# Kernel tuning notes

Measured on AMD Instinct MI355X. Metric: run time of the kernel, lower is better.

The kernel has to match this reference:

```python
import jax, jax.numpy as jnp
import numpy as np

N = 50000      # nodes
E = 300000     # edges per hop
H = 64         # hidden_channels
P = 3          # hops
DIRS = 3
L = 2          # num_layers
G = 50         # graphs in batch
FUS_IN = H * (2 + 2 * DIRS)  # 512
SLOPE = 0.01   # torch leaky_relu default negative slope


def setup_inputs():
    key = jax.random.key(0)
    ks = jax.random.split(key, 32)
    def nrm(k, shape, s=0.1):
        return jax.random.normal(k, shape, jnp.float32) * s
    return {
        "x": jax.random.normal(ks[0], (N, H), jnp.float32),
        "pe": jax.random.normal(ks[1], (N, DIRS), jnp.float32),
        "batch": jnp.sort(jax.random.randint(ks[2], (N,), 0, G, jnp.int32)),
        "u_edge_index": jax.random.randint(ks[3], (P, 2, E), 0, N, jnp.int32),
        "u_edge_weight": jax.random.uniform(ks[4], (P, E), jnp.float32),
        "f_edge_index": jax.random.randint(ks[5], (P, 2, E), 0, N, jnp.int32),
        "f_edge_weight": jax.random.uniform(ks[6], (P, E), jnp.float32),
        "emb_W": nrm(ks[7], (H, H)), "emb_b": nrm(ks[8], (H,)),
        "S_lin_W": nrm(ks[9], (L, H, H)), "S_lin_b": nrm(ks[10], (L, H)),
        "S_d": nrm(ks[11], (L, P, H), 1.0), "S_hb": nrm(ks[12], (L, P, H)),
        "S_fW": nrm(ks[13], (L, P, FUS_IN, H), 0.04), "S_fb": nrm(ks[14], (L, P, H)),
        "F_lin_W": nrm(ks[15], (L, H, H)), "F_lin_b": nrm(ks[16], (L, H)),
        "F_d": nrm(ks[17], (L, P, H), 1.0), "F_hb": nrm(ks[18], (L, P, H)),
        "F_fW": nrm(ks[19], (L, P, FUS_IN, H), 0.04), "F_fb": nrm(ks[20], (L, P, H)),
        "nS_w": 1.0 + nrm(ks[21], (L, H)), "nS_b": nrm(ks[22], (L, H)),
        "nS_m": 1.0 + nrm(ks[23], (L, H)),
        "nF_w": 1.0 + nrm(ks[24], (L, H)), "nF_b": nrm(ks[25], (L, H)),
        "nF_m": 1.0 + nrm(ks[26], (L, H)),
        "gate_W": nrm(ks[27], (2 * H, H)), "gate_b": nrm(ks[28], (H,)),
    }


def _opdmp(x, pe, ei, ew, lin_W, lin_b, d, hop_bias, fus_W, fus_b):
    """One OPDMPConv: multi-hop gather / scatter_add with directional weights."""
    x_t = x @ lin_W + lin_b              # [N, H]
    d_w = jax.nn.softmax(d, axis=0)      # [P, H]
    out = jnp.zeros_like(x_t)
    u = pe[:, :DIRS]
    for p in range(P):
        row, col, w = ei[p, 0], ei[p, 1], ew[p]
        # precompute() runs under torch.no_grad() -> stop_gradient
        deg = jax.ops.segment_sum(jax.lax.stop_gradient(w), row, num_segments=N)
        deg_inv = jnp.where(deg == 0.0, 0.0, 1.0 / deg)                  # [N]
        diff = jax.lax.stop_gradient(u[col] - u[row])                    # [E, DIRS]
        W2 = jnp.concatenate([jax.nn.relu(diff), jax.nn.relu(-diff)], axis=1)  # [E, 2*DIRS]
        xc = x_t[col]                                                    # [E, H] gather
        out_avg = jax.ops.segment_sum(xc * w[:, None], row, num_segments=N) * deg_inv[:, None]
        msg_dir = (xc[:, :, None] * W2[:, None, :]).reshape(E, H * 2 * DIRS)
        out_dir = jax.ops.segment_sum(msg_dir, row, num_segments=N) * deg_inv[:, None]
        h_cat = jnp.concatenate([x_t, out_avg, out_dir], axis=-1)        # [N, FUS_IN]
        h_p = jax.nn.leaky_relu(h_cat @ fus_W[p] + fus_b[p], SLOPE)
        out = out + h_p * d_w[p] + hop_bias[p]
    return out


def _graph_norm(x, batch, w, b, ms):
    cnt = jnp.maximum(jax.ops.segment_sum(jnp.ones((N,), x.dtype), batch, num_segments=G), 1.0)
    mean = jax.ops.segment_sum(x, batch, num_segments=G) / cnt[:, None]
    out = x - mean[batch] * ms
    var = jax.ops.segment_sum(out * out, batch, num_segments=G) / cnt[:, None]
    return out / jnp.sqrt(var[batch] + 1e-5) * w + b


def _forward(x, pe, u_edge_weight, f_edge_weight, emb_W, emb_b,
             S_lin_W, S_lin_b, S_d, S_hb, S_fW, S_fb,
             F_lin_W, F_lin_b, F_d, F_hb, F_fW, F_fb,
             nS_w, nS_b, nS_m, nF_w, nF_b, nF_m,
             gate_W, gate_b, batch, u_edge_index, f_edge_index):
    x = x @ emb_W + emb_b
    for i in range(L):
        prev = x
        h = _opdmp(x, pe, u_edge_index, u_edge_weight,
                   S_lin_W[i], S_lin_b[i], S_d[i], S_hb[i], S_fW[i], S_fb[i])
        h = jax.nn.leaky_relu(_graph_norm(h, batch, nS_w[i], nS_b[i], nS_m[i]), SLOPE)
        fx = _opdmp(h, pe, f_edge_index, f_edge_weight,
                    F_lin_W[i], F_lin_b[i], F_d[i], F_hb[i], F_fW[i], F_fb[i])
        fx = jax.nn.leaky_relu(_graph_norm(fx, batch, nF_w[i], nF_b[i], nF_m[i]), SLOPE)
        gate = jax.nn.sigmoid(jnp.concatenate([h, fx], axis=-1) @ gate_W + gate_b)
        x = gate * h + (1.0 - gate) * fx + prev   # dropout = identity in eval mode
    cnt = jnp.maximum(jax.ops.segment_sum(jnp.ones((N,), x.dtype), batch, num_segments=G), 1.0)
    return jax.ops.segment_sum(x, batch, num_segments=G) / cnt[:, None]  # global_mean_pool


def reference(x, pe, batch, u_edge_index, u_edge_weight, f_edge_index, f_edge_weight,
              emb_W, emb_b, S_lin_W, S_lin_b, S_d, S_hb, S_fW, S_fb,
              F_lin_W, F_lin_b, F_d, F_hb, F_fW, F_fb,
              nS_w, nS_b, nS_m, nF_w, nF_b, nF_m, gate_W, gate_b):
    return _forward(x, pe, u_edge_weight, f_edge_weight, emb_W, emb_b,
                    S_lin_W, S_lin_b, S_d, S_hb, S_fW, S_fb,
                    F_lin_W, F_lin_b, F_d, F_hb, F_fW, F_fb,
                    nS_w, nS_b, nS_m, nF_w, nF_b, nF_m,
                    gate_W, gate_b, batch, u_edge_index, f_edge_index)
```

## Files before the change

kernel.cpp:

```cpp
#include <hip/hip_runtime.h>
#include <cstdint>
#include <cstddef>

#define NN 50000
#define EE 300000
#define HH 64
#define PP 3
#define GG 50
#define LL 2
#define CAP 32
#define SLOPE 0.01f

typedef __attribute__((ext_vector_type(8))) short bf16x8;
typedef __attribute__((ext_vector_type(4))) float f32x4;

__device__ __forceinline__ float lrelu(float x){ return x >= 0.f ? x : SLOPE*x; }

__device__ __forceinline__ unsigned short f2bf(float x){
    uint32_t u = __float_as_uint(x);
    uint32_t r = (u + 0x7FFFu + ((u >> 16) & 1u)) >> 16;
    return (unsigned short)r;
}
__device__ __forceinline__ float bf2f(unsigned short s){
    return __uint_as_float((uint32_t)s << 16);
}

__global__ void k_bounds(const int* __restrict__ batch, int* __restrict__ gstart){
    int g = threadIdx.x;
    if (g > GG) return;
    int lo = 0, hi = NN;
    while (lo < hi){ int mid = (lo + hi) >> 1; if (batch[mid] < g) lo = mid + 1; else hi = mid; }
    gstart[g] = lo;
}

__global__ void k_pe4(const float* __restrict__ pe, float4* __restrict__ pe4){
    int n = blockIdx.x * blockDim.x + threadIdx.x;
    if (n >= NN) return;
    pe4[n] = make_float4(pe[n * 3 + 0], pe[n * 3 + 1], pe[n * 3 + 2], 0.f);
}

__global__ void k_fill2(const int* __restrict__ uei, const float* __restrict__ uew,
                        const int* __restrict__ fei, const float* __restrict__ few,
                        int* __restrict__ cnt, int2* __restrict__ bucket){
    int t = blockIdx.x * blockDim.x + threadIdx.x;
    if (t >= 2 * PP * EE) return;
    int which = t / EE;
    int e = t - which * EE;
    const int* ei; const float* ew; int p;
    if (which < PP){ ei = uei; ew = uew; p = which; }
    else           { ei = fei; ew = few; p = which - PP; }
    int row = ei[(size_t)(p * 2 + 0) * EE + e];
    int col = ei[(size_t)(p * 2 + 1) * EE + e];
    float w = ew[(size_t)p * EE + e];
    int slot = atomicAdd(cnt + (size_t)which * NN + row, 1);
    if (slot < CAP)
        bucket[((size_t)which * NN + row) * CAP + slot] = make_int2(col, __float_as_int(w));
}

__global__ void k_wpermb(const float* __restrict__ S_fW, const float* __restrict__ F_fW,
                         unsigned short* __restrict__ Wpb){
    int gid = blockIdx.x * blockDim.x + threadIdx.x;
    int j = gid & 7;
    int lane = (gid >> 3) & 63;
    int w = (gid >> 9) & 3;
    int kb = (gid >> 11) & 15;
    int t = gid >> 15;
    int q = kb * 32 + (lane >> 4) * 8 + j;
    int col = w * 16 + (lane & 15);
    int conv = t / 6, layer = (t % 6) / 3, p = t % 3;
    const float* src = (conv ? F_fW : S_fW) + ((size_t)layer * PP + p) * 512 * HH;
    int kref;
    if (q < 128) kref = q;
    else { int r = q - 128; kref = 128 + (r & 63) * 6 + (r >> 6); }
    Wpb[gid] = f2bf(src[(size_t)kref * HH + col]);
}

__global__ __launch_bounds__(256) void k_lin64(const float* __restrict__ X,
                       const float* __restrict__ W, const float* __restrict__ b,
                       float* __restrict__ out){
    __shared__ float xs[32][HH];
    int nb = blockIdx.x * 32;
    int t = threadIdx.x;
    #pragma unroll
    for (int i = 0; i < 2; ++i){
        int idx = t + 256 * i;
        int r = idx >> 4, c4 = idx & 15;
        int n = nb + r;
        float4 v = make_float4(0.f, 0.f, 0.f, 0.f);
        if (n < NN) v = *reinterpret_cast<const float4*>(X + (size_t)n * HH + c4 * 4);
        *reinterpret_cast<float4*>(&xs[r][c4 * 4]) = v;
    }
    __syncthreads();
    int lane = t & 63, wave = t >> 6, nw = wave * 8;
    float acc[8];
    float bb = b[lane];
    #pragma unroll
    for (int i = 0; i < 8; ++i) acc[i] = bb;
    #pragma unroll 2
    for (int k = 0; k < HH; ++k){
        float wv = W[(size_t)k * HH + lane];
        #pragma unroll
        for (int i = 0; i < 8; ++i) acc[i] += xs[nw + i][k] * wv;
    }
    #pragma unroll
    for (int i = 0; i < 8; ++i){
        int n = nb + nw + i;
        if (n < NN) out[(size_t)n * HH + lane] = acc[i];
    }
}

__global__ __launch_bounds__(256) void k_lin64b(const float* __restrict__ X,
                       const float* __restrict__ W, const float* __restrict__ b,
                       unsigned short* __restrict__ out){
    __shared__ float xs[32][HH];
    int nb = blockIdx.x * 32;
    int t = threadIdx.x;
    #pragma unroll
    for (int i = 0; i < 2; ++i){
        int idx = t + 256 * i;
        int r = idx >> 4, c4 = idx & 15;
        int n = nb + r;
        float4 v = make_float4(0.f, 0.f, 0.f, 0.f);
        if (n < NN) v = *reinterpret_cast<const float4*>(X + (size_t)n * HH + c4 * 4);
        *reinterpret_cast<float4*>(&xs[r][c4 * 4]) = v;
    }
    __syncthreads();
    int lane = t & 63, wave = t >> 6, nw = wave * 8;
    float acc[8];
    float bb = b[lane];
    #pragma unroll
    for (int i = 0; i < 8; ++i) acc[i] = bb;
    #pragma unroll 2
    for (int k = 0; k < HH; ++k){
        float wv = W[(size_t)k * HH + lane];
        #pragma unroll
        for (int i = 0; i < 8; ++i) acc[i] += xs[nw + i][k] * wv;
    }
    #pragma unroll
    for (int i = 0; i < 8; ++i){
        int n = nb + nw + i;
        if (n < NN) out[(size_t)n * HH + lane] = f2bf(acc[i]);
    }
}

__global__ __launch_bounds__(256) void k_hop3(const unsigned short* __restrict__ xtb,
        const int* __restrict__ cnt, const int2* __restrict__ bucket,
        const float4* __restrict__ pe4, const unsigned short* __restrict__ Wpb3,
        const float* __restrict__ fb3, const float* __restrict__ dmat,
        const float* __restrict__ hb3, float* __restrict__ outb){
    __shared__ unsigned short u[16][512];
    int nb = blockIdx.x * 16;
    int t = threadIdx.x;
    int lane = t & 63, wave = t >> 6, nw = wave * 4;
    {
        int r = t >> 4, c4 = t & 15;
        ushort4 s = *reinterpret_cast<const ushort4*>(xtb + (size_t)(nb + r) * HH + c4 * 4);
        int q = (c4 * 4) ^ ((r & 7) << 3);
        *reinterpret_cast<ushort4*>(&u[r][q]) = s;
    }
    int c = wave * 16 + (lane & 15);
    float d0 = dmat[c], d1 = dmat[64 + c], d2 = dmat[128 + c];
    float mx = fmaxf(d0, fmaxf(d1, d2));
    float e0 = expf(d0 - mx), e1 = expf(d1 - mx), e2 = expf(d2 - mx);
    float esum = e0 + e1 + e2;
    float dw0 = e0 / esum, dw1 = e1 / esum, dw2 = e2 / esum;
    float accOut[4];
    float hbs = hb3[c] + hb3[64 + c] + hb3[128 + c];
    #pragma unroll
    for (int r = 0; r < 4; ++r) accOut[r] = hbs;

    for (int p = 0; p < 3; ++p){
        __syncthreads();
        const int*  cntp = cnt + (size_t)p * NN;
        const int2* bp   = bucket + (size_t)p * NN * CAP;
        #pragma unroll
        for (int i = 0; i < 4; ++i){
            int n = nb + nw + i;
            float accA = 0.f, sumw = 0.f;
            float a0 = 0.f, a1 = 0.f, a2 = 0.f, a3 = 0.f, a4 = 0.f, a5 = 0.f;
            int len = cntp[n]; if (len > CAP) len = CAP;
            const int2* b = bp + (size_t)n * CAP;
            float4 pr = pe4[n];
            {
                int  cols[8]; float ws[8];
                #pragma unroll
                for (int s = 0; s < 8; ++s){
                    int2 m = b[s];
                    bool ok = (s < len);
                    cols[s] = ok ? m.x : n;
                    ws[s]   = ok ? __int_as_float(m.y) : 0.f;
                }
                float4 pcs[8]; float xvs[8];
                #pragma unroll
                for (int s = 0; s < 8; ++s){
                    pcs[s] = pe4[cols[s]];
                    xvs[s] = bf2f(xtb[(size_t)cols[s] * HH + lane]);
                }
                #pragma unroll
                for (int s = 0; s < 8; ++s){
                    float w = ws[s], xv = xvs[s];
                    float dd0 = pcs[s].x - pr.x;
                    float dd1 = pcs[s].y - pr.y;
                    float dd2 = pcs[s].z - pr.z;
                    sumw += w;  accA += w * xv;
                    a0 += fmaxf(dd0, 0.f) * xv;  a3 += fmaxf(-dd0, 0.f) * xv;
                    a1 += fmaxf(dd1, 0.f) * xv;  a4 += fmaxf(-dd1, 0.f) * xv;
                    a2 += fmaxf(dd2, 0.f) * xv;  a5 += fmaxf(-dd2, 0.f) * xv;
                }
            }
            if (len > 8){
                int  cols[8]; float ws[8];
                #pragma unroll
                for (int s = 0; s < 8; ++s){
                    int2 m = b[8 + s];
                    bool ok = (8 + s < len);
                    cols[s] = ok ? m.x : n;
                    ws[s]   = ok ? __int_as_float(m.y) : 0.f;
                }
                float4 pcs[8]; float xvs[8];
                #pragma unroll
                for (int s = 0; s < 8; ++s){
                    pcs[s] = pe4[cols[s]];
                    xvs[s] = bf2f(xtb[(size_t)cols[s] * HH + lane]);
                }
                #pragma unroll
                for (int s = 0; s < 8; ++s){
                    float w = ws[s], xv = xvs[s];
                    float dd0 = pcs[s].x - pr.x;
                    float dd1 = pcs[s].y - pr.y;
                    float dd2 = pcs[s].z - pr.z;
                    sumw += w;  accA += w * xv;
                    a0 += fmaxf(dd0, 0.f) * xv;  a3 += fmaxf(-dd0, 0.f) * xv;
                    a1 += fmaxf(dd1, 0.f) * xv;  a4 += fmaxf(-dd1, 0.f) * xv;
                    a2 += fmaxf(dd2, 0.f) * xv;  a5 += fmaxf(-dd2, 0.f) * xv;
                }
            }
            for (int s = 16; s < len; ++s){
                int2 m = b[s];
                int col = m.x;
                float w = __int_as_float(m.y);
                float4 pc = pe4[col];
                float xv = bf2f(xtb[(size_t)col * HH + lane]);
                float dd0 = pc.x - pr.x;
                float dd1 = pc.y - pr.y;
                float dd2 = pc.z - pr.z;
                sumw += w;  accA += w * xv;
                a0 += fmaxf(dd0, 0.f) * xv;  a3 += fmaxf(-dd0, 0.f) * xv;
                a1 += fmaxf(dd1, 0.f) * xv;  a4 += fmaxf(-dd1, 0.f) * xv;
                a2 += fmaxf(dd2, 0.f) * xv;  a5 += fmaxf(-dd2, 0.f) * xv;
            }
            float di = (sumw == 0.f) ? 0.f : 1.f / sumw;
            int il = nw + i;
            int sw = (il & 7) << 3;
            u[il][(64 + lane) ^ sw]           = f2bf(accA * di);
            u[il][(128 + 0 * 64 + lane) ^ sw] = f2bf(a0 * di);
            u[il][(128 + 1 * 64 + lane) ^ sw] = f2bf(a1 * di);
            u[il][(128 + 2 * 64 + lane) ^ sw] = f2bf(a2 * di);
            u[il][(128 + 3 * 64 + lane) ^ sw] = f2bf(a3 * di);
            u[il][(128 + 4 * 64 + lane) ^ sw] = f2bf(a4 * di);
            u[il][(128 + 5 * 64 + lane) ^ sw] = f2bf(a5 * di);
        }
        __syncthreads();
        const unsigned short* wb = Wpb3 + (size_t)p * 32768;
        f32x4 acc = {0.f, 0.f, 0.f, 0.f};
        int arow = lane & 15;
        int asw = (arow & 7) << 3;
        #pragma unroll
        for (int kb = 0; kb < 16; ++kb){
            int qa = (kb * 32 + (lane >> 4) * 8) ^ asw;
            bf16x8 a = *reinterpret_cast<const bf16x8*>(&u[arow][qa]);
            bf16x8 b = *reinterpret_cast<const bf16x8*>(&wb[(((size_t)kb * 4 + wave) * 64 + lane) * 8]);
            acc = __builtin_amdgcn_mfma_f32_16x16x32_bf16(a, b, acc, 0, 0, 0);
        }
        float fbv = fb3[p * 64 + c];
        float dw = (p == 0) ? dw0 : ((p == 1) ? dw1 : dw2);
        #pragma unroll
        for (int r = 0; r < 4; ++r)
            accOut[r] += lrelu(acc[r] + fbv) * dw;
    }
    #pragma unroll
    for (int r = 0; r < 4; ++r){
        int row = (lane >> 4) * 4 + r;
        outb[(size_t)(nb + row) * HH + c] = accOut[r];
    }
}

__global__ void k_stats4(const float* __restrict__ X, const int* __restrict__ gstart,
                         float* __restrict__ sums4, float* __restrict__ sumsq4){
    int g = blockIdx.x, chunk = blockIdx.y;
    int o = threadIdx.x & 63, sub = threadIdx.x >> 6;
    int ns = gstart[g], ne = gstart[g + 1];
    float s = 0.f, q = 0.f;
    for (int n = ns + chunk * 4 + sub; n < ne; n += 16){
        float v = X[(size_t)n * 64 + o];
        s += v; q += v * v;
    }
    __shared__ float ls[4][64];
    __shared__ float lq[4][64];
    ls[sub][o] = s; lq[sub][o] = q;
    __syncthreads();
    if (sub == 0){
        #pragma unroll
        for (int k = 1; k < 4; ++k){ s += ls[k][o]; q += lq[k][o]; }
        sums4 [(size_t)(chunk * GG + g) * 64 + o] = s;
        sumsq4[(size_t)(chunk * GG + g) * 64 + o] = q;
    }
}

__global__ void k_gnorm(float* __restrict__ X, const int* __restrict__ batch,
                        const int* __restrict__ gstart,
                        const float* __restrict__ sums4, const float* __restrict__ sumsq4,
                        const float* __restrict__ w, const float* __restrict__ b,
                        const float* __restrict__ ms){
    int gid = blockIdx.x * blockDim.x + threadIdx.x;
    if (gid >= NN * HH) return;
    int n = gid >> 6, o = gid & 63;
    int g = batch[n];
    float cnt = fmaxf((float)(gstart[g + 1] - gstart[g]), 1.f);
    float sm = 0.f, sq = 0.f;
    #pragma unroll
    for (int cC = 0; cC < 4; ++cC){
        sm += sums4 [(size_t)(cC * GG + g) * 64 + o];
        sq += sumsq4[(size_t)(cC * GG + g) * 64 + o];
    }
    float mean = sm / cnt;
    float ex2 = sq / cnt;
    float m = ms[o];
    float var = ex2 - mean * mean * m * (2.f - m);
    float v = (X[gid] - mean * m) * (1.f / sqrtf(var + 1e-5f)) * w[o] + b[o];
    X[gid] = lrelu(v);
}

__global__ __launch_bounds__(256) void k_gate2(const float* __restrict__ h,
                       const float* __restrict__ fx, const float* __restrict__ gW,
                       const float* __restrict__ gb, float* __restrict__ X){
    __shared__ float hs[32][HH];
    __shared__ float fs[32][HH];
    int nb = blockIdx.x * 32;
    int t = threadIdx.x;
    #pragma unroll
    for (int i = 0; i < 2; ++i){
        int idx = t + 256 * i;
        int r = idx >> 4, c4 = idx & 15;
        int n = nb + r;
        float4 vh = make_float4(0.f, 0.f, 0.f, 0.f);
        float4 vf = make_float4(0.f, 0.f, 0.f, 0.f);
        if (n < NN){
            vh = *reinterpret_cast<const float4*>(h  + (size_t)n * HH + c4 * 4);
            vf = *reinterpret_cast<const float4*>(fx + (size_t)n * HH + c4 * 4);
        }
        *reinterpret_cast<float4*>(&hs[r][c4 * 4]) = vh;
        *reinterpret_cast<float4*>(&fs[r][c4 * 4]) = vf;
    }
    __syncthreads();
    int lane = t & 63, wave = t >> 6, nw = wave * 8;
    float acc[8];
    float bb = gb[lane];
    #pragma unroll
    for (int i = 0; i < 8; ++i) acc[i] = bb;
    #pragma unroll 2
    for (int k = 0; k < HH; ++k){
        float w1 = gW[(size_t)k * HH + lane];
        float w2 = gW[(size_t)(64 + k) * HH + lane];
        #pragma unroll
        for (int i = 0; i < 8; ++i) acc[i] += hs[nw + i][k] * w1 + fs[nw + i][k] * w2;
    }
    #pragma unroll
    for (int i = 0; i < 8; ++i){
        int n = nb + nw + i;
        if (n < NN){
            float gt = 1.f / (1.f + expf(-acc[i]));
            float hv = hs[nw + i][lane];
            float fv = fs[nw + i][lane];
            size_t idx = (size_t)n * HH + lane;
            X[idx] = gt * hv + (1.f - gt) * fv + X[idx];
        }
    }
}

__global__ void k_finalout(const float* __restrict__ sums4, const int* __restrict__ gstart,
                           float* __restrict__ out){
    int gid = blockIdx.x * blockDim.x + threadIdx.x;
    if (gid >= GG * HH) return;
    int g = gid >> 6, o = gid & 63;
    float cnt = fmaxf((float)(gstart[g + 1] - gstart[g]), 1.f);
    float sm = 0.f;
    #pragma unroll
    for (int cC = 0; cC < 4; ++cC) sm += sums4[(size_t)(cC * GG + g) * 64 + o];
    out[gid] = sm / cnt;
}

extern "C" void kernel_launch(void* const* d_in, const int* in_sizes, int n_in,
                              void* d_out, int out_size, void* d_ws, size_t ws_size,
                              hipStream_t stream) {
    const float* x_in   = (const float*)d_in[0];
    const float* pe     = (const float*)d_in[1];
    const int*   batch  = (const int*)d_in[2];
    const int*   uei    = (const int*)d_in[3];
    const float* uew    = (const float*)d_in[4];
    const int*   fei    = (const int*)d_in[5];
    const float* few    = (const float*)d_in[6];
    const float* emb_W  = (const float*)d_in[7];
    const float* emb_b  = (const float*)d_in[8];
    const float* S_lin_W= (const float*)d_in[9];
    const float* S_lin_b= (const float*)d_in[10];
    const float* S_d    = (const float*)d_in[11];
    const float* S_hb   = (const float*)d_in[12];
    const float* S_fW   = (const float*)d_in[13];
    const float* S_fb   = (const float*)d_in[14];
    const float* F_lin_W= (const float*)d_in[15];
    const float* F_lin_b= (const float*)d_in[16];
    const float* F_d    = (const float*)d_in[17];
    const float* F_hb   = (const float*)d_in[18];
    const float* F_fW   = (const float*)d_in[19];
    const float* F_fb   = (const float*)d_in[20];
    const float* nS_w   = (const float*)d_in[21];
    const float* nS_b   = (const float*)d_in[22];
    const float* nS_m   = (const float*)d_in[23];
    const float* nF_w   = (const float*)d_in[24];
    const float* nF_b   = (const float*)d_in[25];
    const float* nF_m   = (const float*)d_in[26];
    const float* gate_W = (const float*)d_in[27];
    const float* gate_b = (const float*)d_in[28];
    float* out = (float*)d_out;

    size_t off = 0;
    auto alloc = [&](size_t bytes)->void*{
        void* p = (char*)d_ws + off;
        off += (bytes + 255) & ~(size_t)255;
        return p;
    };
    float*  xbuf   = (float*)alloc((size_t)NN * HH * 4);
    float*  hbuf   = (float*)alloc((size_t)NN * HH * 4);
    float*  fxbuf  = (float*)alloc((size_t)NN * HH * 4);
    unsigned short* xtb = (unsigned short*)alloc((size_t)NN * HH * 2);
    unsigned short* Wpb12 = (unsigned short*)alloc((size_t)12 * 32768 * 2);
    float4* pe4    = (float4*)alloc((size_t)NN * 16);
    int*    cnt    = (int*)  alloc((size_t)6 * NN * 4);
    int2*   bucket = (int2*) alloc((size_t)6 * NN * CAP * 8);
    int*    gstart = (int*)  alloc((GG + 1) * 4);
    float*  sums4  = (float*)alloc((size_t)4 * GG * HH * 4);
    float*  sumsq4 = (float*)alloc((size_t)4 * GG * HH * 4);

    const int BLK = 256;
    const int gridNH = (NN * HH) / BLK;
    const int gridN32 = (NN + 31) / 32;
    const int gridHop = NN / 16;
    const int gridEdges = (2 * PP * EE + BLK - 1) / BLK;
    const int gridWb = (12 * 32768) / BLK;

    k_bounds<<<1, 64, 0, stream>>>(batch, gstart);
    k_pe4<<<(NN + BLK - 1) / BLK, BLK, 0, stream>>>(pe, pe4);
    hipMemsetAsync(cnt, 0, (size_t)6 * NN * 4, stream);
    k_fill2<<<gridEdges, BLK, 0, stream>>>(uei, uew, fei, few, cnt, bucket);
    k_wpermb<<<gridWb, BLK, 0, stream>>>(S_fW, F_fW, Wpb12);
    k_lin64<<<gridN32, BLK, 0, stream>>>(x_in, emb_W, emb_b, xbuf);

    auto gnorm = [&](float* X, const float* w, const float* b, const float* ms){
        k_stats4<<<dim3(GG, 4), BLK, 0, stream>>>(X, gstart, sums4, sumsq4);
        k_gnorm<<<gridNH, BLK, 0, stream>>>(X, batch, gstart, sums4, sumsq4, w, b, ms);
    };

    for (int i = 0; i < LL; ++i){
        k_lin64b<<<gridN32, BLK, 0, stream>>>(xbuf, S_lin_W + (size_t)i * HH * HH,
                                              S_lin_b + (size_t)i * HH, xtb);
        k_hop3<<<gridHop, BLK, 0, stream>>>(xtb, cnt, bucket, pe4,
                Wpb12 + (size_t)(0 * 6 + i * 3) * 32768,
                S_fb + (size_t)i * PP * HH, S_d + (size_t)i * PP * HH,
                S_hb + (size_t)i * PP * HH, hbuf);
        gnorm(hbuf, nS_w + (size_t)i * HH, nS_b + (size_t)i * HH, nS_m + (size_t)i * HH);
        k_lin64b<<<gridN32, BLK, 0, stream>>>(hbuf, F_lin_W + (size_t)i * HH * HH,
                                              F_lin_b + (size_t)i * HH, xtb);
        k_hop3<<<gridHop, BLK, 0, stream>>>(xtb, cnt + (size_t)PP * NN,
                bucket + (size_t)PP * NN * CAP, pe4,
                Wpb12 + (size_t)(1 * 6 + i * 3) * 32768,
                F_fb + (size_t)i * PP * HH, F_d + (size_t)i * PP * HH,
                F_hb + (size_t)i * PP * HH, fxbuf);
        gnorm(fxbuf, nF_w + (size_t)i * HH, nF_b + (size_t)i * HH, nF_m + (size_t)i * HH);
        k_gate2<<<gridN32, BLK, 0, stream>>>(hbuf, fxbuf, gate_W, gate_b, xbuf);
    }

    k_stats4<<<dim3(GG, 4), BLK, 0, stream>>>(xbuf, gstart, sums4, sumsq4);
    k_finalout<<<(GG * HH + BLK - 1) / BLK, BLK, 0, stream>>>(sums4, gstart, out);
}
```

Before: 1.032 ms.

## Fold graph-norm apply into consumer linear and gate kernels via per-graph scale/shift

Replaces the standalone in-place graph-norm kernel with a tiny per-graph kernel that computes scale and shift, then applies normalisation plus leaky-relu on load inside the following linear kernel and the gate kernel. This removes four full read-modify-write passes over the N×64 float activations per forward. In exchange the gate kernel re-applies the norm to both inputs and does extra per-row batch and scale/shift loads, and hbuf now holds unnormalised values that later consumers must treat consistently.

```diff
diff --git a/kernel.cpp b/kernel.cpp
--- a/kernel.cpp
+++ b/kernel.cpp
@@ -123,6 +123,52 @@
         float4 v = make_float4(0.f, 0.f, 0.f, 0.f);
         if (n < NN) v = *reinterpret_cast<const float4*>(X + (size_t)n * HH + c4 * 4);
         *reinterpret_cast<float4*>(&xs[r][c4 * 4]) = v;
+    }
+    __syncthreads();
+    int lane = t & 63, wave = t >> 6, nw = wave * 8;
+    float acc[8];
+    float bb = b[lane];
+    #pragma unroll
+    for (int i = 0; i < 8; ++i) acc[i] = bb;
+    #pragma unroll 2
+    for (int k = 0; k < HH; ++k){
+        float wv = W[(size_t)k * HH + lane];
+        #pragma unroll
+        for (int i = 0; i < 8; ++i) acc[i] += xs[nw + i][k] * wv;
+    }
+    #pragma unroll
+    for (int i = 0; i < 8; ++i){
+        int n = nb + nw + i;
+        if (n < NN) out[(size_t)n * HH + lane] = f2bf(acc[i]);
+    }
+}
+
+__global__ __launch_bounds__(256) void k_lin64bg(const float* __restrict__ X,
+                       const int* __restrict__ batch,
+                       const float* __restrict__ scale, const float* __restrict__ shift,
+                       const float* __restrict__ W, const float* __restrict__ b,
+                       unsigned short* __restrict__ out){
+    __shared__ float xs[32][HH];
+    int nb = blockIdx.x * 32;
+    int t = threadIdx.x;
+    #pragma unroll
+    for (int i = 0; i < 2; ++i){
+        int idx = t + 256 * i;
+        int r = idx >> 4, c4 = idx & 15;
+        int n = nb + r;
+        if (n < NN){
+            int g = batch[n];
+            float4 v = *reinterpret_cast<const float4*>(X + (size_t)n * HH + c4 * 4);
+            float4 sc = *reinterpret_cast<const float4*>(scale + (size_t)g * HH + c4 * 4);
+            float4 sh = *reinterpret_cast<const float4*>(shift + (size_t)g * HH + c4 * 4);
+            v.x = lrelu(v.x * sc.x + sh.x);
+            v.y = lrelu(v.y * sc.y + sh.y);
+            v.z = lrelu(v.z * sc.z + sh.z);
+            v.w = lrelu(v.w * sc.w + sh.w);
+            *reinterpret_cast<float4*>(&xs[r][c4 * 4]) = v;
+        } else {
+            *reinterpret_cast<float4*>(&xs[r][c4 * 4]) = make_float4(0.f,0.f,0.f,0.f);
+        }
     }
     __syncthreads();
     int lane = t & 63, wave = t >> 6, nw = wave * 8;
@@ -307,15 +353,12 @@
     }
 }
 
-__global__ void k_gnorm(float* __restrict__ X, const int* __restrict__ batch,
-                        const int* __restrict__ gstart,
-                        const float* __restrict__ sums4, const float* __restrict__ sumsq4,
-                        const float* __restrict__ w, const float* __restrict__ b,
-                        const float* __restrict__ ms){
-    int gid = blockIdx.x * blockDim.x + threadIdx.x;
-    if (gid >= NN * HH) return;
-    int n = gid >> 6, o = gid & 63;
-    int g = batch[n];
+__global__ void k_prep(const int* __restrict__ gstart,
+                       const float* __restrict__ sums4, const float* __restrict__ sumsq4,
+                       const float* __restrict__ w, const float* __restrict__ b,
+                       const float* __restrict__ ms,
+                       float* __restrict__ scale, float* __restrict__ shift){
+    int g = blockIdx.x, o = threadIdx.x;
     float cnt = fmaxf((float)(gstart[g + 1] - gstart[g]), 1.f);
     float sm = 0.f, sq = 0.f;
     #pragma unroll
@@ -327,13 +370,17 @@
     float ex2 = sq / cnt;
     float m = ms[o];
     float var = ex2 - mean * mean * m * (2.f - m);
-    float v = (X[gid] - mean * m) * (1.f / sqrtf(var + 1e-5f)) * w[o] + b[o];
-    X[gid] = lrelu(v);
-}
-
-__global__ __launch_bounds__(256) void k_gate2(const float* __restrict__ h,
-                       const float* __restrict__ fx, const float* __restrict__ gW,
-                       const float* __restrict__ gb, float* __restrict__ X){
+    float sc = (1.f / sqrtf(var + 1e-5f)) * w[o];
+    scale[g * HH + o] = sc;
+    shift[g * HH + o] = b[o] - mean * m * sc;
+}
+
+__global__ __launch_bounds__(256) void k_gate2g(const float* __restrict__ h,
+                       const float* __restrict__ fx, const int* __restrict__ batch,
+                       const float* __restrict__ scS, const float* __restrict__ shS,
+                       const float* __restrict__ scF, const float* __restrict__ shF,
+                       const float* __restrict__ gW, const float* __restrict__ gb,
+                       float* __restrict__ X){
     __shared__ float hs[32][HH];
     __shared__ float fs[32][HH];
     int nb = blockIdx.x * 32;
@@ -343,14 +390,24 @@
         int idx = t + 256 * i;
         int r = idx >> 4, c4 = idx & 15;
         int n = nb + r;
-        float4 vh = make_float4(0.f, 0.f, 0.f, 0.f);
-        float4 vf = make_float4(0.f, 0.f, 0.f, 0.f);
         if (n < NN){
-            vh = *reinterpret_cast<const float4*>(h  + (size_t)n * HH + c4 * 4);
-            vf = *reinterpret_cast<const float4*>(fx + (size_t)n * HH + c4 * 4);
+            int g = batch[n];
+            float4 vh = *reinterpret_cast<const float4*>(h  + (size_t)n * HH + c4 * 4);
+            float4 vf = *reinterpret_cast<const float4*>(fx + (size_t)n * HH + c4 * 4);
+            float4 s1 = *reinterpret_cast<const float4*>(scS + (size_t)g * HH + c4 * 4);
+            float4 h1 = *reinterpret_cast<const float4*>(shS + (size_t)g * HH + c4 * 4);
+            float4 s2 = *reinterpret_cast<const float4*>(scF + (size_t)g * HH + c4 * 4);
+            float4 h2 = *reinterpret_cast<const float4*>(shF + (size_t)g * HH + c4 * 4);
+            vh.x = lrelu(vh.x * s1.x + h1.x); vh.y = lrelu(vh.y * s1.y + h1.y);
+            vh.z = lrelu(vh.z * s1.z + h1.z); vh.w = lrelu(vh.w * s1.w + h1.w);
+            vf.x = lrelu(vf.x * s2.x + h2.x); vf.y = lrelu(vf.y * s2.y + h2.y);
+            vf.z = lrelu(vf.z * s2.z + h2.z); vf.w = lrelu(vf.w * s2.w + h2.w);
+            *reinterpret_cast<float4*>(&hs[r][c4 * 4]) = vh;
+            *reinterpret_cast<float4*>(&fs[r][c4 * 4]) = vf;
+        } else {
+            *reinterpret_cast<float4*>(&hs[r][c4 * 4]) = make_float4(0.f,0.f,0.f,0.f);
+            *reinterpret_cast<float4*>(&fs[r][c4 * 4]) = make_float4(0.f,0.f,0.f,0.f);
         }
-        *reinterpret_cast<float4*>(&hs[r][c4 * 4]) = vh;
-        *reinterpret_cast<float4*>(&fs[r][c4 * 4]) = vf;
     }
     __syncthreads();
     int lane = t & 63, wave = t >> 6, nw = wave * 8;
@@ -441,9 +498,12 @@
     int*    gstart = (int*)  alloc((GG + 1) * 4);
     float*  sums4  = (float*)alloc((size_t)4 * GG * HH * 4);
     float*  sumsq4 = (float*)alloc((size_t)4 * GG * HH * 4);
+    float*  scS    = (float*)alloc(GG * HH * 4);
+    float*  shS    = (float*)alloc(GG * HH * 4);
+    float*  scF    = (float*)alloc(GG * HH * 4);
+    float*  shF    = (float*)alloc(GG * HH * 4);
 
     const int BLK = 256;
-    const int gridNH = (NN * HH) / BLK;
     const int gridN32 = (NN + 31) / 32;
     const int gridHop = NN / 16;
     const int gridEdges = (2 * PP * EE + BLK - 1) / BLK;
@@ -455,11 +515,6 @@
     k_fill2<<<gridEdges, BLK, 0, stream>>>(uei, uew, fei, few, cnt, bucket);
     k_wpermb<<<gridWb, BLK, 0, stream>>>(S_fW, F_fW, Wpb12);
     k_lin64<<<gridN32, BLK, 0, stream>>>(x_in, emb_W, emb_b, xbuf);
-
-    auto gnorm = [&](float* X, const float* w, const float* b, const float* ms){
-        k_stats4<<<dim3(GG, 4), BLK, 0, stream>>>(X, gstart, sums4, sumsq4);
-        k_gnorm<<<gridNH, BLK, 0, stream>>>(X, batch, gstart, sums4, sumsq4, w, b, ms);
-    };
 
     for (int i = 0; i < LL; ++i){
         k_lin64b<<<gridN32, BLK, 0, stream>>>(xbuf, S_lin_W + (size_t)i * HH * HH,
@@ -468,16 +523,24 @@
                 Wpb12 + (size_t)(0 * 6 + i * 3) * 32768,
                 S_fb + (size_t)i * PP * HH, S_d + (size_t)i * PP * HH,
                 S_hb + (size_t)i * PP * HH, hbuf);
-        gnorm(hbuf, nS_w + (size_t)i * HH, nS_b + (size_t)i * HH, nS_m + (size_t)i * HH);
-        k_lin64b<<<gridN32, BLK, 0, stream>>>(hbuf, F_lin_W + (size_t)i * HH * HH,
-                                              F_lin_b + (size_t)i * HH, xtb);
+        k_stats4<<<dim3(GG, 4), BLK, 0, stream>>>(hbuf, gstart, sums4, sumsq4);
+        k_prep<<<GG, 64, 0, stream>>>(gstart, sums4, sumsq4,
+                nS_w + (size_t)i * HH, nS_b + (size_t)i * HH, nS_m + (size_t)i * HH,
+                scS, shS);
+        k_lin64bg<<<gridN32, BLK, 0, stream>>>(hbuf, batch, scS, shS,
+                                               F_lin_W + (size_t)i * HH * HH,
+                                               F_lin_b + (size_t)i * HH, xtb);
         k_hop3<<<gridHop, BLK, 0, stream>>>(xtb, cnt + (size_t)PP * NN,
                 bucket + (size_t)PP * NN * CAP, pe4,
                 Wpb12 + (size_t)(1 * 6 + i * 3) * 32768,
                 F_fb + (size_t)i * PP * HH, F_d + (size_t)i * PP * HH,
                 F_hb + (size_t)i * PP * HH, fxbuf);
-        gnorm(fxbuf, nF_w + (size_t)i * HH, nF_b + (size_t)i * HH, nF_m + (size_t)i * HH);
-        k_gate2<<<gridN32, BLK, 0, stream>>>(hbuf, fxbuf, gate_W, gate_b, xbuf);
+        k_stats4<<<dim3(GG, 4), BLK, 0, stream>>>(fxbuf, gstart, sums4, sumsq4);
+        k_prep<<<GG, 64, 0, stream>>>(gstart, sums4, sumsq4,
+                nF_w + (size_t)i * HH, nF_b + (size_t)i * HH, nF_m + (size_t)i * HH,
+                scF, shF);
+        k_gate2g<<<gridN32, BLK, 0, stream>>>(hbuf, fxbuf, batch, scS, shS, scF, shF,
+                                              gate_W, gate_b, xbuf);
     }
 
     k_stats4<<<dim3(GG, 4), BLK, 0, stream>>>(xbuf, gstart, sums4, sumsq4);
```

After: 985.6 us. -4.5%, faster.
